# Kernel optimization log

Measured on AMD Instinct MI355X. Metric: run time of the kernel, lower is better.

## Reference

```python
import jax, jax.numpy as jnp
import numpy as np

B, L_IN, F = 64, 256, 64
N_EXO = 16
N_ENDO = F - N_EXO
H = 1024
L_OUT = 64


def _lstm_params(key, in_dim, hid):
    k = 1.0 / np.sqrt(hid)
    k1, k2, k3, k4 = jax.random.split(key, 4)
    Wih = jax.random.uniform(k1, (4 * hid, in_dim), jnp.float32, -k, k)
    Whh = jax.random.uniform(k2, (4 * hid, hid), jnp.float32, -k, k)
    bih = jax.random.uniform(k3, (4 * hid,), jnp.float32, -k, k)
    bhh = jax.random.uniform(k4, (4 * hid,), jnp.float32, -k, k)
    return Wih, Whh, bih, bhh


def setup_inputs() -> dict:
    key = jax.random.key(0)
    ks = jax.random.split(key, 8)
    src = jax.random.normal(ks[0], (B, L_IN, F), jnp.float32)
    trg = jax.random.normal(ks[1], (B, L_OUT, F), jnp.float32)
    eW0 = _lstm_params(ks[2], F, H)
    eW1 = _lstm_params(ks[3], H, H)
    dW0 = _lstm_params(ks[4], F, H)  # decoder input size = n_endo + n_exo = F
    dW1 = _lstm_params(ks[5], H, H)
    kf = 1.0 / np.sqrt(H)
    fc_W = jax.random.uniform(ks[6], (N_ENDO, H), jnp.float32, -kf, kf)
    fc_b = jax.random.uniform(ks[7], (N_ENDO,), jnp.float32, -kf, kf)
    return {
        'src': src, 'trg': trg,
        'enc_Wih0': eW0[0], 'enc_Whh0': eW0[1], 'enc_bih0': eW0[2], 'enc_bhh0': eW0[3],
        'enc_Wih1': eW1[0], 'enc_Whh1': eW1[1], 'enc_bih1': eW1[2], 'enc_bhh1': eW1[3],
        'dec_Wih0': dW0[0], 'dec_Whh0': dW0[1], 'dec_bih0': dW0[2], 'dec_bhh0': dW0[3],
        'dec_Wih1': dW1[0], 'dec_Whh1': dW1[1], 'dec_bih1': dW1[2], 'dec_bhh1': dW1[3],
        'fc_W': fc_W, 'fc_b': fc_b,
    }


def _cell(x, h, c, Wih, Whh, bih, bhh):
    # torch gate order: i, f, g, o
    gates = x @ Wih.T + h @ Whh.T + (bih + bhh)
    i, f, g, o = jnp.split(gates, 4, axis=-1)
    c_new = jax.nn.sigmoid(f) * c + jax.nn.sigmoid(i) * jnp.tanh(g)
    h_new = jax.nn.sigmoid(o) * jnp.tanh(c_new)
    return h_new, c_new


def reference(src, trg,
              enc_Wih0, enc_Whh0, enc_bih0, enc_bhh0,
              enc_Wih1, enc_Whh1, enc_bih1, enc_bhh1,
              dec_Wih0, dec_Whh0, dec_bih0, dec_bhh0,
              dec_Wih1, dec_Whh1, dec_bih1, dec_bhh1,
              fc_W, fc_b):
    b = src.shape[0]
    z = jnp.zeros((b, H), src.dtype)

    # ---- encoder: 2-layer LSTM over src time dim ----
    def enc_step(carry, x_t):
        h0, c0, h1, c1 = carry
        h0, c0 = _cell(x_t, h0, c0, enc_Wih0, enc_Whh0, enc_bih0, enc_bhh0)
        h1, c1 = _cell(h0, h1, c1, enc_Wih1, enc_Whh1, enc_bih1, enc_bhh1)
        return (h0, c0, h1, c1), None

    (h0, c0, h1, c1), _ = jax.lax.scan(enc_step, (z, z, z, z),
                                       jnp.swapaxes(src, 0, 1))  # [L_in, B, F]

    exo = jnp.swapaxes(trg[:, :, N_ENDO:], 0, 1)  # [L_out, B, n_exo]
    dec_in0 = src[:, -1, :]

    def dec_step(carry, exo_t):
        h0, c0, h1, c1, x = carry
        h0, c0 = _cell(x, h0, c0, dec_Wih0, dec_Whh0, dec_bih0, dec_bhh0)
        h1, c1 = _cell(h0, h1, c1, dec_Wih1, dec_Whh1, dec_bih1, dec_bhh1)
        pred = h1 @ fc_W.T + fc_b  # [B, n_endo]
        x_next = jnp.concatenate([pred, exo_t], axis=1)
        return (h0, c0, h1, c1, x_next), pred

    _, preds = jax.lax.scan(dec_step, (h0, c0, h1, c1, dec_in0), exo)
    return jnp.swapaxes(preds, 0, 1)  # [B, L_out, n_endo]
```

## Files before the change

kernel.cpp:

```cpp
#include <hip/hip_runtime.h>
#include <math.h>

#define LIN 256
#define LOUT 64
#define NENDO 48

typedef __attribute__((ext_vector_type(8))) short short8;
typedef __attribute__((ext_vector_type(4))) float f32x4;
typedef __attribute__((ext_vector_type(16))) float f32x16;

constexpr size_t O_APE0 = 0;
constexpr size_t O_APE1 = 17825792;
constexpr size_t O_APD0 = 51380224;
constexpr size_t O_APD1 = 69206016;
constexpr size_t O_SRCF = 102760448;
constexpr size_t O_EXH  = 106954752;
constexpr size_t O_EXL  = 107085824;
constexpr size_t O_H0F  = 107216896;
constexpr size_t O_H1F  = 107741184;
constexpr size_t O_XF   = 108265472;
constexpr size_t O_H1KM = 108298240;
constexpr size_t O_BIAS = 108560384;
constexpr size_t O_BAR  = 108625920;

__device__ __forceinline__ unsigned short f2bh(float x) {
    unsigned int u = __float_as_uint(x);
    unsigned int r = (u + 0x7fffu + ((u >> 16) & 1u)) >> 16;
    return (unsigned short)r;
}
__device__ __forceinline__ float bh2f(unsigned short h) {
    return __uint_as_float(((unsigned int)h) << 16);
}
__device__ __forceinline__ float sigf(float x) { return 1.0f / (1.0f + expf(-x)); }

__device__ __forceinline__ void load4_cc(const unsigned short* base,
                                         short8& h0, short8& l0, short8& h1, short8& l1)
{
    asm volatile(
        "global_load_dwordx4 %0, %4, off sc0 sc1\n\t"
        "global_load_dwordx4 %1, %4, off offset:1024 sc0 sc1\n\t"
        "global_load_dwordx4 %2, %4, off offset:2048 sc0 sc1\n\t"
        "global_load_dwordx4 %3, %4, off offset:3072 sc0 sc1"
        : "=&v"(h0), "=&v"(l0), "=&v"(h1), "=&v"(l1)
        : "v"(base)
        : "memory");
}
__device__ __forceinline__ void store_us_cc(unsigned short* p, unsigned short v) {
    unsigned int w = v;
    asm volatile("global_store_short %0, %1, off sc0 sc1" :: "v"(p), "v"(w) : "memory");
}
__device__ __forceinline__ void store_f_cc(float* p, float v) {
    asm volatile("global_store_dword %0, %1, off sc0 sc1" :: "v"(p), "v"(v) : "memory");
}
__device__ __forceinline__ void load_f_cc_issue(const float* p, float& dst) {
    asm volatile("global_load_dword %0, %1, off sc0 sc1" : "=v"(dst) : "v"(p) : "memory");
}

__device__ __forceinline__ size_t frag_off(int k, int b, int spl) {
    return (size_t)(k >> 4) * 2048 + (size_t)(b >> 5) * 1024 + (size_t)spl * 512
         + (size_t)((b & 31) + 32 * ((k >> 3) & 1)) * 8 + (k & 7);
}

__global__ void pack_a32(const float* __restrict__ Wx, const float* __restrict__ Wh,
                         unsigned short* __restrict__ out, int KX, int NC)
{
    const int n = 128 * NC * 512;
    for (int j = blockIdx.x * blockDim.x + threadIdx.x; j < n; j += gridDim.x * blockDim.x) {
        int r2 = j & 511;
        int c = (j >> 9) % NC;
        int T = (j >> 9) / NC;
        int l = r2 >> 3, e = r2 & 7;
        int p = T * 32 + (l & 31);
        int hcol = p >> 2, gate = p & 3;
        int k = c * 16 + (l >> 5) * 8 + e;
        float v = (k < KX) ? Wx[(gate * 1024 + hcol) * KX + k]
                           : Wh[(gate * 1024 + hcol) * 1024 + (k - KX)];
        unsigned short h = f2bh(v);
        size_t o = ((size_t)(T * NC + c) * 2) * 512 + r2;
        out[o] = h;
        out[o + 512] = f2bh(v - bh2f(h));
    }
}

__global__ void pack_bias_kernel(const float* a0, const float* b0, const float* a1, const float* b1,
                                 const float* a2, const float* b2, const float* a3, const float* b3,
                                 float* d)
{
    int i = blockIdx.x * blockDim.x + threadIdx.x;
    if (i >= 4096) return;
    int hcol = i >> 2, gate = i & 3, s = (gate << 10) + hcol;
    d[i] = a0[s] + b0[s];
    d[4096 + i] = a1[s] + b1[s];
    d[8192 + i] = a2[s] + b2[s];
    d[12288 + i] = a3[s] + b3[s];
}

__global__ void prep_misc(const float* __restrict__ src, const float* __restrict__ trg,
                          char* __restrict__ wsb)
{
    unsigned short* hz = (unsigned short*)(wsb + O_H0F);
    int* bar = (int*)(wsb + O_BAR);
    unsigned short* srcf = (unsigned short*)(wsb + O_SRCF);
    unsigned short* exh = (unsigned short*)(wsb + O_EXH);
    unsigned short* exl = (unsigned short*)(wsb + O_EXL);
    unsigned short* xf0 = (unsigned short*)(wsb + O_XF);
    const int N0 = 524288, N1 = 2048, N2 = 1048576, N3 = 65536, N4 = 4096;
    const int TOT = N0 + N1 + N2 + N3 + N4;
    for (int i = blockIdx.x * blockDim.x + threadIdx.x; i < TOT; i += gridDim.x * blockDim.x) {
        if (i < N0) {
            hz[i] = 0;
        } else if (i < N0 + N1) {
            bar[i - N0] = 0;
        } else if (i < N0 + N1 + N2) {
            int j = i - (N0 + N1);
            int t = j >> 12, b = (j >> 6) & 63, k = j & 63;
            float v = src[(b * LIN + t) * 64 + k];
            unsigned short h = f2bh(v);
            unsigned short* d = srcf + (size_t)t * 8192;
            d[frag_off(k, b, 0)] = h;
            d[frag_off(k, b, 1)] = f2bh(v - bh2f(h));
        } else if (i < N0 + N1 + N2 + N3) {
            int j = i - (N0 + N1 + N2);
            int t = j >> 10, b = (j >> 4) & 63, e = j & 15;
            float v = trg[(b * LOUT + t) * 64 + NENDO + e];
            unsigned short h = f2bh(v);
            exh[j] = h; exl[j] = f2bh(v - bh2f(h));
        } else {
            int j = i - (N0 + N1 + N2 + N3);
            int b = j >> 6, k = j & 63;
            float v = src[(b * LIN + (LIN - 1)) * 64 + k];
            unsigned short h = f2bh(v);
            xf0[frag_off(k, b, 0)] = h;
            xf0[frag_off(k, b, 1)] = f2bh(v - bh2f(h));
        }
    }
}

template <int CNT>
__device__ __forceinline__ void load_a(const unsigned short* __restrict__ ap, int T, int NC,
                                       int base, int l, short8* A)
{
#pragma unroll
    for (int i = 0; i < CNT; i++) {
#pragma unroll
        for (int s = 0; s < 2; s++)
            A[i * 2 + s] = *(const short8*)(ap + (((size_t)T * NC + (base + i)) * 2 + s) * 512 + l * 8);
    }
}

template <int CNT>
__device__ __forceinline__ void compute_ph(const unsigned short* __restrict__ B1, int S,
                                           const unsigned short* __restrict__ B2,
                                           int base, const short8* A, int l,
                                           f32x16& a0, f32x16& a1)
{
    short8 bh0[2], bl0[2], bh1[2], bl1[2];
    auto addr = [&](int i) -> const unsigned short* {
        int ks = base + i;
        const unsigned short* fb = (ks < S) ? (B1 + (size_t)ks * 2048) : (B2 + (size_t)(ks - S) * 2048);
        return fb + l * 8;
    };
    load4_cc(addr(0), bh0[0], bl0[0], bh1[0], bl1[0]);
    __builtin_amdgcn_sched_barrier(0);
#pragma unroll
    for (int i = 0; i < CNT; i++) {
        const int cur = i & 1, nxt = cur ^ 1;
        if (i + 1 < CNT) {
            load4_cc(addr(i + 1), bh0[nxt], bl0[nxt], bh1[nxt], bl1[nxt]);
            __builtin_amdgcn_sched_barrier(0);
            asm volatile("s_waitcnt vmcnt(4)" ::: "memory");
        } else {
            asm volatile("s_waitcnt vmcnt(0)" ::: "memory");
        }
        __builtin_amdgcn_sched_barrier(0);
        short8 ah = A[i * 2], al = A[i * 2 + 1];
        a0 = __builtin_amdgcn_mfma_f32_32x32x16_bf16(ah, bh0[cur], a0, 0, 0, 0);
        a1 = __builtin_amdgcn_mfma_f32_32x32x16_bf16(ah, bh1[cur], a1, 0, 0, 0);
        a0 = __builtin_amdgcn_mfma_f32_32x32x16_bf16(ah, bl0[cur], a0, 0, 0, 0);
        a1 = __builtin_amdgcn_mfma_f32_32x32x16_bf16(ah, bl1[cur], a1, 0, 0, 0);
        a0 = __builtin_amdgcn_mfma_f32_32x32x16_bf16(al, bh0[cur], a0, 0, 0, 0);
        a1 = __builtin_amdgcn_mfma_f32_32x32x16_bf16(al, bh1[cur], a1, 0, 0, 0);
        __builtin_amdgcn_sched_barrier(0);
    }
}

__device__ __forceinline__ void reduce_epi(float* ldsf, f32x16& a0, f32x16& a1,
                                           int w, int l, int T,
                                           const float* __restrict__ biasP,
                                           unsigned short* __restrict__ Hout,
                                           float* __restrict__ km, float* creg)
{
    const int l31 = l & 31, l5 = l >> 5;
    __syncthreads();
#pragma unroll
    for (int j = 0; j < 16; j++) {
        ldsf[((w * 2 + 0) * 16 + j) * 64 + l] = a0[j];
        ldsf[((w * 2 + 1) * 16 + j) * 64 + l] = a1[j];
    }
    __syncthreads();
    if (w < 2) {
#pragma unroll
        for (int q = 0; q < 4; q++) {
            float gv[4];
#pragma unroll
            for (int j = 0; j < 4; j++) {
                float v = 0.0f;
#pragma unroll
                for (int kt = 0; kt < 8; kt++) v += ldsf[((kt * 2 + w) * 16 + (q * 4 + j)) * 64 + l];
                gv[j] = v;
            }
            int hcol = T * 8 + 2 * q + l5;
            int b = w * 32 + l31;
            const f32x4 bv = *(const f32x4*)(biasP + hcol * 4);
            float ig = sigf(gv[0] + bv[0]);
            float fg = sigf(gv[1] + bv[1]);
            float gg = tanhf(gv[2] + bv[2]);
            float og = sigf(gv[3] + bv[3]);
            float cv = fg * creg[q] + ig * gg;
            creg[q] = cv;
            float hv = og * tanhf(cv);
            if (km) store_f_cc(km + hcol * 64 + b, hv);
            unsigned short hh = f2bh(hv);
            unsigned short hl = f2bh(hv - bh2f(hh));
            size_t fo = (size_t)(T >> 1) * 2048 + (size_t)w * 1024
                      + (size_t)(l31 + 32 * (T & 1)) * 8 + (2 * q + l5);
            store_us_cc(Hout + fo, hh);
            store_us_cc(Hout + fo + 512, hl);
        }
    }
}

__device__ __forceinline__ void gridbar(int* bar, int& ep, int tid)
{
    asm volatile("s_waitcnt vmcnt(0)" ::: "memory");
    __syncthreads();
    ep++;
    if (tid == 0) {
        int a = __hip_atomic_fetch_add(&bar[0], 1, __ATOMIC_RELAXED, __HIP_MEMORY_SCOPE_AGENT);
        if (a == ep * 256 - 1)
            __hip_atomic_store(&bar[256], ep, __ATOMIC_RELAXED, __HIP_MEMORY_SCOPE_AGENT);
        while (__hip_atomic_load(&bar[256], __ATOMIC_RELAXED, __HIP_MEMORY_SCOPE_AGENT) < ep)
            __builtin_amdgcn_s_sleep(2);
    }
    __syncthreads();
}

__global__ __launch_bounds__(512, 2) void persist(char* __restrict__ wsb,
                                                  const float* __restrict__ fcW,
                                                  const float* __restrict__ fcb,
                                                  float* __restrict__ out)
{
    __shared__ float ldsf[16384];

    const unsigned short* apE0 = (const unsigned short*)(wsb + O_APE0);
    const unsigned short* apE1 = (const unsigned short*)(wsb + O_APE1);
    const unsigned short* apD0 = (const unsigned short*)(wsb + O_APD0);
    const unsigned short* apD1 = (const unsigned short*)(wsb + O_APD1);
    const unsigned short* srcf = (const unsigned short*)(wsb + O_SRCF);
    const unsigned short* exh = (const unsigned short*)(wsb + O_EXH);
    const unsigned short* exl = (const unsigned short*)(wsb + O_EXL);
    unsigned short* h0f[2] = { (unsigned short*)(wsb + O_H0F), (unsigned short*)(wsb + O_H0F + 262144) };
    unsigned short* h1f[2] = { (unsigned short*)(wsb + O_H1F), (unsigned short*)(wsb + O_H1F + 262144) };
    unsigned short* xf[2] = { (unsigned short*)(wsb + O_XF), (unsigned short*)(wsb + O_XF + 16384) };
    float* h1km = (float*)(wsb + O_H1KM);
    const float* biasB = (const float*)(wsb + O_BIAS);
    int* bar = (int*)(wsb + O_BAR);

    const int tid = threadIdx.x;
    const int l = tid & 63;
    const int w = tid >> 6;
    const int g = blockIdx.x;
    const bool isL0 = g < 128;
    const int T = isL0 ? g : g - 128;
    const int base0 = (w < 4) ? w * 9 : 36 + (w - 4) * 8;
    int ep = 0;

    short8 Areg[32];
    float creg[4] = {0.f, 0.f, 0.f, 0.f};

    if (isL0) {
        if (w < 4) load_a<9>(apE0, T, 68, base0, l, Areg);
        else       load_a<8>(apE0, T, 68, base0, l, Areg);
    } else {
        load_a<16>(apE1, T, 128, w * 16, l, Areg);
    }

    for (int d = 0; d <= LIN; d++) {
        if (isL0) {
            if (d < LIN) {
                f32x16 a0 = {}, a1 = {};
                const unsigned short* B1 = srcf + (size_t)d * 8192;
                const unsigned short* B2 = h0f[(d + 1) & 1];
                if (w < 4) compute_ph<9>(B1, 4, B2, base0, Areg, l, a0, a1);
                else       compute_ph<8>(B1, 4, B2, base0, Areg, l, a0, a1);
                reduce_epi(ldsf, a0, a1, w, l, T, biasB, h0f[d & 1], nullptr, creg);
            }
        } else {
            if (d >= 1) {
                f32x16 a0 = {}, a1 = {};
                const unsigned short* B1 = h0f[(d + 1) & 1];
                const unsigned short* B2 = h1f[(d + 1) & 1];
                compute_ph<16>(B1, 64, B2, w * 16, Areg, l, a0, a1);
                reduce_epi(ldsf, a0, a1, w, l, T, biasB + 4096, h1f[d & 1], nullptr, creg);
            }
        }
        gridbar(bar, ep, tid);
    }

    if (isL0) {
        if (w < 4) load_a<9>(apD0, T, 68, base0, l, Areg);
        else       load_a<8>(apD0, T, 68, base0, l, Areg);
    } else {
        load_a<16>(apD1, T, 128, w * 16, l, Areg);
    }

    for (int t = 0; t < LOUT; t++) {
        if (isL0) {
            f32x16 a0 = {}, a1 = {};
            const unsigned short* B1 = xf[t & 1];
            const unsigned short* B2 = h0f[(t + 1) & 1];
            if (w < 4) compute_ph<9>(B1, 4, B2, base0, Areg, l, a0, a1);
            else       compute_ph<8>(B1, 4, B2, base0, Areg, l, a0, a1);
            reduce_epi(ldsf, a0, a1, w, l, T, biasB + 8192, h0f[t & 1], nullptr, creg);
        }
        gridbar(bar, ep, tid);

        if (!isL0) {
            f32x16 a0 = {}, a1 = {};
            const unsigned short* B1 = h0f[t & 1];
            const unsigned short* B2 = h1f[t & 1];
            compute_ph<16>(B1, 64, B2, w * 16, Areg, l, a0, a1);
            reduce_epi(ldsf, a0, a1, w, l, T, biasB + 12288, h1f[(t + 1) & 1], h1km, creg);
        }
        gridbar(bar, ep, tid);

        if (g < NENDO) {
            const int b_ = tid & 63, kw = tid >> 6;
            const float* hp = h1km + b_;
            const float* wp = fcW + g * 1024 + kw * 128;
            float vb[2][32];
            float acc = 0.0f;
#pragma unroll
            for (int u = 0; u < 32; u++)
                load_f_cc_issue(hp + (size_t)(kw * 128 + u) * 64, vb[0][u]);
            __builtin_amdgcn_sched_barrier(0);
#pragma unroll
            for (int j = 0; j < 4; j++) {
                if (j + 1 < 4) {
#pragma unroll
                    for (int u = 0; u < 32; u++)
                        load_f_cc_issue(hp + (size_t)(kw * 128 + (j + 1) * 32 + u) * 64, vb[(j + 1) & 1][u]);
                    __builtin_amdgcn_sched_barrier(0);
                    asm volatile("s_waitcnt vmcnt(32)" ::: "memory");
                } else {
                    asm volatile("s_waitcnt vmcnt(0)" ::: "memory");
                }
                __builtin_amdgcn_sched_barrier(0);
#pragma unroll
                for (int u = 0; u < 32; u++)
                    acc = fmaf(vb[j & 1][u], wp[j * 32 + u], acc);
            }
            __syncthreads();
            ldsf[kw * 64 + b_] = acc;
            __syncthreads();
            if (tid < 64) {
                float s = fcb[g];
#pragma unroll
                for (int j = 0; j < 8; j++) s += ldsf[j * 64 + tid];
                out[tid * (LOUT * NENDO) + t * NENDO + g] = s;
                unsigned short hh = f2bh(s);
                unsigned short hl = f2bh(s - bh2f(hh));
                unsigned short* x2 = xf[(t + 1) & 1];
                store_us_cc(x2 + frag_off(g, tid, 0), hh);
                store_us_cc(x2 + frag_off(g, tid, 1), hl);
            }
        } else if (g == NENDO) {
#pragma unroll
            for (int r = 0; r < 2; r++) {
                int idx = tid + r * 512;
                int e = idx >> 6, b = idx & 63;
                int k = NENDO + e;
                unsigned short* x2 = xf[(t + 1) & 1];
                store_us_cc(x2 + frag_off(k, b, 0), exh[t * 1024 + b * 16 + e]);
                store_us_cc(x2 + frag_off(k, b, 1), exl[t * 1024 + b * 16 + e]);
            }
        }
        gridbar(bar, ep, tid);
    }
}

extern "C" void kernel_launch(void* const* d_in, const int* in_sizes, int n_in,
                              void* d_out, int out_size, void* d_ws, size_t ws_size,
                              hipStream_t stream)
{
    const float* src = (const float*)d_in[0];
    const float* trg = (const float*)d_in[1];
    const float* eWih0 = (const float*)d_in[2];
    const float* eWhh0 = (const float*)d_in[3];
    const float* ebih0 = (const float*)d_in[4];
    const float* ebhh0 = (const float*)d_in[5];
    const float* eWih1 = (const float*)d_in[6];
    const float* eWhh1 = (const float*)d_in[7];
    const float* ebih1 = (const float*)d_in[8];
    const float* ebhh1 = (const float*)d_in[9];
    const float* dWih0 = (const float*)d_in[10];
    const float* dWhh0 = (const float*)d_in[11];
    const float* dbih0 = (const float*)d_in[12];
    const float* dbhh0 = (const float*)d_in[13];
    const float* dWih1 = (const float*)d_in[14];
    const float* dWhh1 = (const float*)d_in[15];
    const float* dbih1 = (const float*)d_in[16];
    const float* dbhh1 = (const float*)d_in[17];
    const float* fcW = (const float*)d_in[18];
    const float* fcb = (const float*)d_in[19];

    char* wsb = (char*)d_ws;
    float* out = (float*)d_out;
    auto U = [&](size_t o) { return (unsigned short*)(wsb + o); };

    pack_a32<<<2048, 256, 0, stream>>>(eWih0, eWhh0, U(O_APE0), 64, 68);
    pack_a32<<<4096, 256, 0, stream>>>(eWih1, eWhh1, U(O_APE1), 1024, 128);
    pack_a32<<<2048, 256, 0, stream>>>(dWih0, dWhh0, U(O_APD0), 64, 68);
    pack_a32<<<4096, 256, 0, stream>>>(dWih1, dWhh1, U(O_APD1), 1024, 128);
    pack_bias_kernel<<<16, 256, 0, stream>>>(ebih0, ebhh0, ebih1, ebhh1,
                                             dbih0, dbhh0, dbih1, dbhh1,
                                             (float*)(wsb + O_BIAS));
    prep_misc<<<1024, 256, 0, stream>>>(src, trg, wsb);

    persist<<<256, 512, 0, stream>>>(wsb, fcW, fcb, out);
}
```

Baseline: 7.360 ms.

## Cache recurrent state loads in L2 with one per-XCD invalidate per grid barrier

Recurrent-state loads (h fragments and h1 for the FC head) drop the sc1 bit, so they may hit in the XCD-local L2 instead of going to memory. To keep this coherent, the grid barrier now elects one workgroup per XCD (found via the XCC_ID hardware register and an atomic max on a per-XCD slot) to run an agent-scope acquire fence. The other workgroups on that XCD wait for a done flag. This adds a second spin stage to every barrier and relies on the fence invalidating L2 for the whole XCD; if it does not, stale data could be read.

```diff
diff --git a/kernel.cpp b/kernel.cpp
--- a/kernel.cpp
+++ b/kernel.cpp
@@ -33,27 +33,28 @@
 }
 __device__ __forceinline__ float sigf(float x) { return 1.0f / (1.0f + expf(-x)); }
 
-__device__ __forceinline__ void load4_cc(const unsigned short* base,
+__device__ __forceinline__ void store_us_cc(unsigned short* p, unsigned short v) {
+    unsigned int w = v;
+    asm volatile("global_store_short %0, %1, off sc0 sc1" :: "v"(p), "v"(w) : "memory");
+}
+__device__ __forceinline__ void store_f_cc(float* p, float v) {
+    asm volatile("global_store_dword %0, %1, off sc0 sc1" :: "v"(p), "v"(v) : "memory");
+}
+
+__device__ __forceinline__ void load4_c0(const unsigned short* base,
                                          short8& h0, short8& l0, short8& h1, short8& l1)
 {
     asm volatile(
-        "global_load_dwordx4 %0, %4, off sc0 sc1\n\t"
-        "global_load_dwordx4 %1, %4, off offset:1024 sc0 sc1\n\t"
-        "global_load_dwordx4 %2, %4, off offset:2048 sc0 sc1\n\t"
-        "global_load_dwordx4 %3, %4, off offset:3072 sc0 sc1"
+        "global_load_dwordx4 %0, %4, off sc0\n\t"
+        "global_load_dwordx4 %1, %4, off offset:1024 sc0\n\t"
+        "global_load_dwordx4 %2, %4, off offset:2048 sc0\n\t"
+        "global_load_dwordx4 %3, %4, off offset:3072 sc0"
         : "=&v"(h0), "=&v"(l0), "=&v"(h1), "=&v"(l1)
         : "v"(base)
         : "memory");
 }
-__device__ __forceinline__ void store_us_cc(unsigned short* p, unsigned short v) {
-    unsigned int w = v;
-    asm volatile("global_store_short %0, %1, off sc0 sc1" :: "v"(p), "v"(w) : "memory");
-}
-__device__ __forceinline__ void store_f_cc(float* p, float v) {
-    asm volatile("global_store_dword %0, %1, off sc0 sc1" :: "v"(p), "v"(v) : "memory");
-}
-__device__ __forceinline__ void load_f_cc_issue(const float* p, float& dst) {
-    asm volatile("global_load_dword %0, %1, off sc0 sc1" : "=v"(dst) : "v"(p) : "memory");
+__device__ __forceinline__ void load_f_c0_issue(const float* p, float& dst) {
+    asm volatile("global_load_dword %0, %1, off sc0" : "=v"(dst) : "v"(p) : "memory");
 }
 
 __device__ __forceinline__ size_t frag_off(int k, int b, int spl) {
@@ -160,13 +161,13 @@
         const unsigned short* fb = (ks < S) ? (B1 + (size_t)ks * 2048) : (B2 + (size_t)(ks - S) * 2048);
         return fb + l * 8;
     };
-    load4_cc(addr(0), bh0[0], bl0[0], bh1[0], bl1[0]);
+    load4_c0(addr(0), bh0[0], bl0[0], bh1[0], bl1[0]);
     __builtin_amdgcn_sched_barrier(0);
 #pragma unroll
     for (int i = 0; i < CNT; i++) {
         const int cur = i & 1, nxt = cur ^ 1;
         if (i + 1 < CNT) {
-            load4_cc(addr(i + 1), bh0[nxt], bl0[nxt], bh1[nxt], bl1[nxt]);
+            load4_c0(addr(i + 1), bh0[nxt], bl0[nxt], bh1[nxt], bl1[nxt]);
             __builtin_amdgcn_sched_barrier(0);
             asm volatile("s_waitcnt vmcnt(4)" ::: "memory");
         } else {
@@ -230,6 +231,12 @@
     }
 }
 
+__device__ __forceinline__ int get_xcc_id() {
+    int x;
+    asm("s_getreg_b32 %0, hwreg(HW_REG_XCC_ID)" : "=s"(x));
+    return x & 7;
+}
+
 __device__ __forceinline__ void gridbar(int* bar, int& ep, int tid)
 {
     asm volatile("s_waitcnt vmcnt(0)" ::: "memory");
@@ -241,6 +248,18 @@
             __hip_atomic_store(&bar[256], ep, __ATOMIC_RELAXED, __HIP_MEMORY_SCOPE_AGENT);
         while (__hip_atomic_load(&bar[256], __ATOMIC_RELAXED, __HIP_MEMORY_SCOPE_AGENT) < ep)
             __builtin_amdgcn_s_sleep(2);
+        const int xcd = get_xcc_id();
+        int* slot = &bar[512 + xcd * 16];
+        int* done = &bar[1024 + xcd * 16];
+        int old = __hip_atomic_fetch_max(slot, ep, __ATOMIC_RELAXED, __HIP_MEMORY_SCOPE_AGENT);
+        if (old < ep) {
+            __builtin_amdgcn_fence(__ATOMIC_ACQUIRE, "agent");
+            asm volatile("s_waitcnt vmcnt(0)" ::: "memory");
+            __hip_atomic_store(done, ep, __ATOMIC_RELAXED, __HIP_MEMORY_SCOPE_AGENT);
+        } else {
+            while (__hip_atomic_load(done, __ATOMIC_RELAXED, __HIP_MEMORY_SCOPE_AGENT) < ep)
+                __builtin_amdgcn_s_sleep(1);
+        }
     }
     __syncthreads();
 }
@@ -342,14 +361,14 @@
             float acc = 0.0f;
 #pragma unroll
             for (int u = 0; u < 32; u++)
-                load_f_cc_issue(hp + (size_t)(kw * 128 + u) * 64, vb[0][u]);
+                load_f_c0_issue(hp + (size_t)(kw * 128 + u) * 64, vb[0][u]);
             __builtin_amdgcn_sched_barrier(0);
 #pragma unroll
             for (int j = 0; j < 4; j++) {
                 if (j + 1 < 4) {
 #pragma unroll
                     for (int u = 0; u < 32; u++)
-                        load_f_cc_issue(hp + (size_t)(kw * 128 + (j + 1) * 32 + u) * 64, vb[(j + 1) & 1][u]);
+                        load_f_c0_issue(hp + (size_t)(kw * 128 + (j + 1) * 32 + u) * 64, vb[(j + 1) & 1][u]);
                     __builtin_amdgcn_sched_barrier(0);
                     asm volatile("s_waitcnt vmcnt(32)" ::: "memory");
                 } else {
@@ -367,7 +386,7 @@
                 float s = fcb[g];
 #pragma unroll
                 for (int j = 0; j < 8; j++) s += ldsf[j * 64 + tid];
-                out[tid * (LOUT * NENDO) + t * NENDO + g] = s;
+                store_f_cc(out + tid * (LOUT * NENDO) + t * NENDO + g, s);
                 unsigned short hh = f2bh(s);
                 unsigned short hl = f2bh(s - bh2f(hh));
                 unsigned short* x2 = xf[(t + 1) & 1];
```

Measured after the change: 7.774 ms. 1.06x slower.
